# Optimization experiments

Measured on AMD Instinct MI355X. Metric: run time of the kernel, lower is better.

## Reference

```python
import jax, jax.numpy as jnp
import numpy as np
import math

N_HEADS = 16


def setup_inputs() -> dict:
    key = jax.random.key(0)
    ks = jax.random.split(key, 5)
    B, S, E = 2, 2048, 1024
    scale = 1.0 / math.sqrt(E)
    return {
        "x": jax.random.normal(ks[0], (B, S, E), dtype=jnp.float32),
        "w_in": jax.random.normal(ks[1], (3 * E, E), dtype=jnp.float32) * scale,
        "b_in": jax.random.normal(ks[2], (3 * E,), dtype=jnp.float32) * 0.01,
        "w_out": jax.random.normal(ks[3], (E, E), dtype=jnp.float32) * scale,
        "b_out": jax.random.normal(ks[4], (E,), dtype=jnp.float32) * 0.01,
    }


def reference(x, w_in, b_in, w_out, b_out):
    B, S, E = x.shape
    H = N_HEADS
    d = E // H
    # fused QKV projection: [B,S,3E]
    qkv = x @ w_in.T + b_in
    q, k, v = jnp.split(qkv, 3, axis=-1)
    # [B,S,E] -> [B,H,S,d]
    q = q.reshape(B, S, H, d).transpose(0, 2, 1, 3)
    k = k.reshape(B, S, H, d).transpose(0, 2, 1, 3)
    v = v.reshape(B, S, H, d).transpose(0, 2, 1, 3)
    # scores [B,H,S,S], scaled by 1/sqrt(d_head) (no causal mask: casual_mask=False)
    scores = jnp.einsum("bhqd,bhkd->bhqk", q, k) / jnp.sqrt(jnp.float32(d)).astype(x.dtype)
    w = jax.nn.softmax(scores, axis=-1)
    # attention output [B,H,S,d] -> [B,S,E]
    out = jnp.einsum("bhqk,bhkd->bhqd", w, v)
    out = out.transpose(0, 2, 1, 3).reshape(B, S, E)
    return out @ w_out.T + b_out
```

## Files before the change

kernel.cpp:

```cpp
#include <hip/hip_runtime.h>
#include <cstdint>


typedef __bf16 bf16x8 __attribute__((ext_vector_type(8)));
typedef short s16x4 __attribute__((ext_vector_type(4)));
typedef float f32x4 __attribute__((ext_vector_type(4)));

__device__ __forceinline__ unsigned short f32_to_bf16_rne(float f) {
    unsigned int u = __builtin_bit_cast(unsigned int, f);
    u += 0x7FFF + ((u >> 16) & 1);
    return (unsigned short)(u >> 16);
}

__device__ __forceinline__ unsigned int pack_bf16_trunc(float a, float b) {
    unsigned int ua = __builtin_bit_cast(unsigned int, a);
    unsigned int ub = __builtin_bit_cast(unsigned int, b);
    return __builtin_amdgcn_perm(ub, ua, 0x07060302u);
}

__device__ __forceinline__ void gload16(const void* g, void* l) {
    __builtin_amdgcn_global_load_lds(
        (const __attribute__((address_space(1))) unsigned int*)g,
        (__attribute__((address_space(3))) unsigned int*)l, 16, 0, 0);
}

__global__ void cvt_all(const float* __restrict__ x, const float* __restrict__ wi,
                        const float* __restrict__ wo, unsigned short* __restrict__ xb,
                        unsigned short* __restrict__ wib, unsigned short* __restrict__ wob) {
    int i = blockIdx.x * blockDim.x + threadIdx.x;
    const float* src; unsigned short* dst; int off;
    if (i < 1048576)            { src = x;  dst = xb;  off = i; }
    else if (i < 1048576 + 786432) { src = wi; dst = wib; off = i - 1048576; }
    else                        { src = wo; dst = wob; off = i - (1048576 + 786432); }
    float4 v = ((const float4*)src)[off];
    ushort4 o;
    o.x = f32_to_bf16_rne(v.x); o.y = f32_to_bf16_rne(v.y);
    o.z = f32_to_bf16_rne(v.z); o.w = f32_to_bf16_rne(v.w);
    ((ushort4*)dst)[off] = o;
}

__launch_bounds__(256)
__global__ void gemm_qkv(const unsigned short* __restrict__ X,
                         const unsigned short* __restrict__ W,
                         const float* __restrict__ bias,
                         unsigned short* __restrict__ Qp,
                         unsigned short* __restrict__ Kp,
                         unsigned short* __restrict__ Vt) {
    __shared__ __align__(16) unsigned short As[128 * 64];
    __shared__ __align__(16) unsigned short Bs[128 * 64];
    const int t = threadIdx.x;
    const int w = t >> 6, lane = t & 63, quad = lane >> 4, l16 = lane & 15;
    const int wm = (w >> 1) * 64, wn = (w & 1) * 64;
    const int m0 = blockIdx.y * 128, n0 = blockIdx.x * 128;

    f32x4 acc[4][4] = {};

    for (int kt = 0; kt < 1024; kt += 64) {
        __syncthreads();
#pragma unroll
        for (int i = 0; i < 4; ++i) {
            int c = t + 256 * i;
            int r = c >> 3, cc = (c & 7) * 8;
            gload16(&X[(m0 + r) * 1024 + kt + cc], &As[c * 8]);
            gload16(&W[(n0 + r) * 1024 + kt + cc], &Bs[c * 8]);
        }
        __syncthreads();
#pragma unroll
        for (int ks = 0; ks < 2; ++ks) {
            bf16x8 af[4], bw[4];
#pragma unroll
            for (int mi = 0; mi < 4; ++mi)
                af[mi] = *(const bf16x8*)&As[(wm + mi * 16 + l16) * 64 + ks * 32 + quad * 8];
#pragma unroll
            for (int ni = 0; ni < 4; ++ni)
                bw[ni] = *(const bf16x8*)&Bs[(wn + ni * 16 + l16) * 64 + ks * 32 + quad * 8];
#pragma unroll
            for (int mi = 0; mi < 4; ++mi)
#pragma unroll
                for (int ni = 0; ni < 4; ++ni)
                    acc[mi][ni] = __builtin_amdgcn_mfma_f32_16x16x32_bf16(af[mi], bw[ni], acc[mi][ni], 0, 0, 0);
        }
    }

    const float QSCALE = 0.125f * 1.44269504089f;
#pragma unroll
    for (int mi = 0; mi < 4; ++mi) {
#pragma unroll
        for (int ni = 0; ni < 4; ++ni) {
            int col = n0 + wn + ni * 16 + l16;
            float bv = bias[col];
            int which = col >> 10;
            int hc = col & 1023;
            int h = hc >> 6, d = hc & 63;
            int row0 = m0 + wm + mi * 16 + quad * 4;
            int b = row0 >> 11, s0 = row0 & 2047;
            int bh = b * 16 + h;
            if (which == 2) {
                ushort4 pk;
                pk.x = f32_to_bf16_rne(acc[mi][ni][0] + bv);
                pk.y = f32_to_bf16_rne(acc[mi][ni][1] + bv);
                pk.z = f32_to_bf16_rne(acc[mi][ni][2] + bv);
                pk.w = f32_to_bf16_rne(acc[mi][ni][3] + bv);
                *(ushort4*)&Vt[(bh * 64 + d) * 2048 + s0] = pk;
            } else if (which == 0) {
#pragma unroll
                for (int r = 0; r < 4; ++r)
                    Qp[(bh * 2048 + s0 + r) * 64 + d] =
                        f32_to_bf16_rne((acc[mi][ni][r] + bv) * QSCALE);
            } else {
#pragma unroll
                for (int r = 0; r < 4; ++r)
                    Kp[(bh * 2048 + s0 + r) * 64 + d] = f32_to_bf16_rne(acc[mi][ni][r] + bv);
            }
        }
    }
}

__launch_bounds__(256, 4)
__global__ void attn(const unsigned short* __restrict__ Qp, const unsigned short* __restrict__ Kp,
                     const unsigned short* __restrict__ Vt, unsigned short* __restrict__ A2) {
    __shared__ __align__(16) unsigned short Ks[2][64 * 64];
    __shared__ __align__(16) unsigned short Vs[2][64 * 64];
    const int t = threadIdx.x, lane = t & 63, quad = lane >> 4, l16 = lane & 15;
    const int w = t >> 6;
    const int wq = w & 1;
    const int wk = w >> 1;
    const int bh = blockIdx.x;
    const int qb = blockIdx.y;
    const unsigned short* Qh = Qp + bh * (2048 * 64);
    const unsigned short* Kh = Kp + bh * (2048 * 64);
    const unsigned short* Vh = Vt + bh * (64 * 2048);

    bf16x8 qf[2][2];
#pragma unroll
    for (int nq = 0; nq < 2; ++nq)
#pragma unroll
        for (int ks = 0; ks < 2; ++ks) {
            int row = qb * 64 + wq * 32 + nq * 16 + l16;
            qf[nq][ks] = *(const bf16x8*)&Qh[row * 64 + ks * 32 + quad * 8];
        }

    f32x4 o_acc[4][2] = {};
    float l_lane[2] = {0.f, 0.f};

#pragma unroll
    for (int i = 0; i < 2; ++i) {
        int c = t + 256 * i;
        int r = c >> 3, sc = ((c & 7) ^ (r & 7)) << 3;
        gload16(&Kh[r * 64 + sc], &Ks[0][c * 8]);
        gload16(&Vh[r * 2048 + sc], &Vs[0][c * 8]);
    }

    int cur = 0;
    for (int it = 0; it < 32; ++it) {
        __syncthreads();
        if (it != 31) {
            int ktn = (it + 1) * 64;
#pragma unroll
            for (int i = 0; i < 2; ++i) {
                int c = t + 256 * i;
                int r = c >> 3, sc = ((c & 7) ^ (r & 7)) << 3;
                gload16(&Kh[(ktn + r) * 64 + sc], &Ks[cur ^ 1][c * 8]);
                gload16(&Vh[r * 2048 + ktn + sc], &Vs[cur ^ 1][c * 8]);
            }
        }
        const unsigned short* Kc = Ks[cur];
        const unsigned short* Vc = Vs[cur];

        f32x4 s_acc[2][2] = {};
#pragma unroll
        for (int ks = 0; ks < 2; ++ks)
#pragma unroll
            for (int mi = 0; mi < 2; ++mi) {
                int row = wk * 32 + mi * 16 + l16;
                bf16x8 kf = *(const bf16x8*)&Kc[row * 64 +
                                                (((ks * 4 + quad) ^ (l16 & 7)) << 3)];
#pragma unroll
                for (int nq = 0; nq < 2; ++nq)
                    s_acc[mi][nq] = __builtin_amdgcn_mfma_f32_16x16x32_bf16(kf, qf[nq][ks], s_acc[mi][nq], 0, 0, 0);
            }

        s16x4 bq[2][2];
#pragma unroll
        for (int nq = 0; nq < 2; ++nq) {
            float rsum = 0.f;
#pragma unroll
            for (int mi = 0; mi < 2; ++mi) {
                float p0 = __builtin_amdgcn_exp2f(s_acc[mi][nq][0]);
                float p1 = __builtin_amdgcn_exp2f(s_acc[mi][nq][1]);
                float p2 = __builtin_amdgcn_exp2f(s_acc[mi][nq][2]);
                float p3 = __builtin_amdgcn_exp2f(s_acc[mi][nq][3]);
                rsum += (p0 + p1) + (p2 + p3);
                uint2 pk;
                pk.x = pack_bf16_trunc(p0, p1);
                pk.y = pack_bf16_trunc(p2, p3);
                bq[mi][nq] = __builtin_bit_cast(s16x4, pk);
            }
            l_lane[nq] += rsum;
        }

#pragma unroll
        for (int dm = 0; dm < 4; ++dm)
#pragma unroll
            for (int kt4 = 0; kt4 < 2; ++kt4) {
                int ch = (wk * 4 + kt4 * 2 + (quad >> 1)) ^ (l16 & 7);
                s16x4 av = __builtin_bit_cast(s16x4,
                    *(const uint2*)&Vc[(dm * 16 + l16) * 64 + (ch << 3) + (quad & 1) * 4]);
#pragma unroll
                for (int nq = 0; nq < 2; ++nq)
                    o_acc[dm][nq] = __builtin_amdgcn_mfma_f32_16x16x16bf16_1k(av, bq[kt4][nq], o_acc[dm][nq], 0, 0, 0);
            }
        cur ^= 1;
    }

    __syncthreads();
    float* fo = (float*)&Ks[0][0];
    float* fl = (float*)&Vs[0][0];
    if (wk == 1) {
#pragma unroll
        for (int nq = 0; nq < 2; ++nq) {
#pragma unroll
            for (int dm = 0; dm < 4; ++dm)
                *(f32x4*)&fo[(wq * 32 + nq * 16 + l16) * 64 + dm * 16 + quad * 4] = o_acc[dm][nq];
            fl[(wq * 2 + nq) * 64 + lane] = l_lane[nq];
        }
    }
    __syncthreads();
    if (wk == 0) {
        const int b = bh >> 4, h = bh & 15;
#pragma unroll
        for (int nq = 0; nq < 2; ++nq) {
#pragma unroll
            for (int dm = 0; dm < 4; ++dm)
                o_acc[dm][nq] += *(const f32x4*)&fo[(wq * 32 + nq * 16 + l16) * 64 + dm * 16 + quad * 4];
            float l = l_lane[nq] + fl[(wq * 2 + nq) * 64 + lane];
            l += __shfl_xor(l, 16);
            l += __shfl_xor(l, 32);
            float rl = 1.0f / l;
            int s = qb * 64 + wq * 32 + nq * 16 + l16;
            int tok = b * 2048 + s;
#pragma unroll
            for (int dm = 0; dm < 4; ++dm) {
                ushort4 o;
                o.x = f32_to_bf16_rne(o_acc[dm][nq][0] * rl);
                o.y = f32_to_bf16_rne(o_acc[dm][nq][1] * rl);
                o.z = f32_to_bf16_rne(o_acc[dm][nq][2] * rl);
                o.w = f32_to_bf16_rne(o_acc[dm][nq][3] * rl);
                *(ushort4*)&A2[tok * 1024 + h * 64 + dm * 16 + quad * 4] = o;
            }
        }
    }
}

__launch_bounds__(256)
__global__ void gemm_out_k(const unsigned short* __restrict__ A, const unsigned short* __restrict__ W,
                           const float* __restrict__ bias, float* __restrict__ out) {
    __shared__ __align__(16) unsigned short As[128 * 64];
    __shared__ __align__(16) unsigned short Bs[64 * 64];
    const int t = threadIdx.x;
    const int w = t >> 6, lane = t & 63, quad = lane >> 4, l16 = lane & 15;
    const int wm = (w >> 1) * 64, wn = (w & 1) * 32;
    const int m0 = blockIdx.y * 128, n0 = blockIdx.x * 64;

    f32x4 acc[4][2] = {};

    for (int kt = 0; kt < 1024; kt += 64) {
        __syncthreads();
#pragma unroll
        for (int i = 0; i < 4; ++i) {
            int c = t + 256 * i;
            int r = c >> 3, cc = (c & 7) * 8;
            gload16(&A[(m0 + r) * 1024 + kt + cc], &As[c * 8]);
        }
#pragma unroll
        for (int i = 0; i < 2; ++i) {
            int c = t + 256 * i;
            int r = c >> 3, cc = (c & 7) * 8;
            gload16(&W[(n0 + r) * 1024 + kt + cc], &Bs[c * 8]);
        }
        __syncthreads();
#pragma unroll
        for (int ks = 0; ks < 2; ++ks) {
            bf16x8 af[4], bw[2];
#pragma unroll
            for (int mi = 0; mi < 4; ++mi)
                af[mi] = *(const bf16x8*)&As[(wm + mi * 16 + l16) * 64 + ks * 32 + quad * 8];
#pragma unroll
            for (int ni = 0; ni < 2; ++ni)
                bw[ni] = *(const bf16x8*)&Bs[(wn + ni * 16 + l16) * 64 + ks * 32 + quad * 8];
#pragma unroll
            for (int mi = 0; mi < 4; ++mi)
#pragma unroll
                for (int ni = 0; ni < 2; ++ni)
                    acc[mi][ni] = __builtin_amdgcn_mfma_f32_16x16x32_bf16(af[mi], bw[ni], acc[mi][ni], 0, 0, 0);
        }
    }

#pragma unroll
    for (int mi = 0; mi < 4; ++mi)
#pragma unroll
        for (int ni = 0; ni < 2; ++ni) {
            int col = n0 + wn + ni * 16 + l16;
            float bv = bias[col];
#pragma unroll
            for (int r = 0; r < 4; ++r) {
                int row = m0 + wm + mi * 16 + quad * 4 + r;
                out[row * 1024 + col] = acc[mi][ni][r] + bv;
            }
        }
}

extern "C" void kernel_launch(void* const* d_in, const int* in_sizes, int n_in,
                              void* d_out, int out_size, void* d_ws, size_t ws_size,
                              hipStream_t stream) {
    const float* x     = (const float*)d_in[0];
    const float* w_in  = (const float*)d_in[1];
    const float* b_in  = (const float*)d_in[2];
    const float* w_out = (const float*)d_in[3];
    const float* b_out = (const float*)d_in[4];
    float* out = (float*)d_out;

    char* ws = (char*)d_ws;
    unsigned short* xb  = (unsigned short*)(ws);
    unsigned short* wib = (unsigned short*)(ws + 8388608);
    unsigned short* wob = (unsigned short*)(ws + 14680064);
    unsigned short* Qp  = (unsigned short*)(ws + 16777216);
    unsigned short* Kp  = (unsigned short*)(ws + 25165824);
    unsigned short* Vt  = (unsigned short*)(ws + 33554432);
    unsigned short* A2  = (unsigned short*)(ws + 41943040);

    cvt_all<<<8192, 256, 0, stream>>>(x, w_in, w_out, xb, wib, wob);
    gemm_qkv<<<dim3(24, 32), 256, 0, stream>>>(xb, wib, b_in, Qp, Kp, Vt);
    attn<<<dim3(32, 32), 256, 0, stream>>>(Qp, Kp, Vt, A2);
    gemm_out_k<<<dim3(16, 32), 256, 0, stream>>>(A2, wob, b_out, out);
}
```

Before: 200.0 us.

## Double-buffer LDS in both projection GEMMs and remap blocks per XCD

Both the QKV and output-projection GEMMs now use two LDS buffers with a K-step of 32. Each iteration prefetches the next tile through global_load_lds while the MFMAs run on the current tile, and only one barrier per step is needed. The launch grids are flattened to 1D and block indices are remapped so that each XCD works on a contiguous sub-grid, which is meant to improve L2 reuse of the shared A and W tiles. The smaller K-step means twice as many barriers and loop iterations, and overlap depends on the barrier's implicit vmcnt wait.

```diff
diff --git a/kernel.cpp b/kernel.cpp
--- a/kernel.cpp
+++ b/kernel.cpp
@@ -46,41 +46,56 @@
                          unsigned short* __restrict__ Qp,
                          unsigned short* __restrict__ Kp,
                          unsigned short* __restrict__ Vt) {
-    __shared__ __align__(16) unsigned short As[128 * 64];
-    __shared__ __align__(16) unsigned short Bs[128 * 64];
+    __shared__ __align__(16) unsigned short As[2][128 * 32];
+    __shared__ __align__(16) unsigned short Bs[2][128 * 32];
     const int t = threadIdx.x;
     const int w = t >> 6, lane = t & 63, quad = lane >> 4, l16 = lane & 15;
     const int wm = (w >> 1) * 64, wn = (w & 1) * 64;
-    const int m0 = blockIdx.y * 128, n0 = blockIdx.x * 128;
-
+    const int lin = blockIdx.x;
+    const int xcd = lin & 7, idx = lin >> 3;
+    const int bx = (xcd & 1) * 12 + idx % 12;
+    const int by = (xcd >> 1) * 8 + idx / 12;
+    const int m0 = by * 128, n0 = bx * 128;
+
+    const int sr = t >> 2, scc = (t & 3) * 8;
     f32x4 acc[4][4] = {};
 
-    for (int kt = 0; kt < 1024; kt += 64) {
+#pragma unroll
+    for (int i = 0; i < 2; ++i) {
+        int c = t + 256 * i;
+        int r = c >> 2, cc = (c & 3) * 8;
+        gload16(&X[(m0 + r) * 1024 + cc], &As[0][c * 8]);
+        gload16(&W[(n0 + r) * 1024 + cc], &Bs[0][c * 8]);
+    }
+
+    int cur = 0;
+    for (int kt = 0; kt < 1024; kt += 32) {
         __syncthreads();
-#pragma unroll
-        for (int i = 0; i < 4; ++i) {
-            int c = t + 256 * i;
-            int r = c >> 3, cc = (c & 7) * 8;
-            gload16(&X[(m0 + r) * 1024 + kt + cc], &As[c * 8]);
-            gload16(&W[(n0 + r) * 1024 + kt + cc], &Bs[c * 8]);
-        }
-        __syncthreads();
-#pragma unroll
-        for (int ks = 0; ks < 2; ++ks) {
-            bf16x8 af[4], bw[4];
-#pragma unroll
-            for (int mi = 0; mi < 4; ++mi)
-                af[mi] = *(const bf16x8*)&As[(wm + mi * 16 + l16) * 64 + ks * 32 + quad * 8];
+        if (kt != 992) {
+            int kn = kt + 32;
+#pragma unroll
+            for (int i = 0; i < 2; ++i) {
+                int c = t + 256 * i;
+                int r = c >> 2, cc = (c & 3) * 8;
+                gload16(&X[(m0 + r) * 1024 + kn + cc], &As[cur ^ 1][c * 8]);
+                gload16(&W[(n0 + r) * 1024 + kn + cc], &Bs[cur ^ 1][c * 8]);
+            }
+        }
+        bf16x8 af[4], bw[4];
+#pragma unroll
+        for (int mi = 0; mi < 4; ++mi)
+            af[mi] = *(const bf16x8*)&As[cur][(wm + mi * 16 + l16) * 32 + quad * 8];
+#pragma unroll
+        for (int ni = 0; ni < 4; ++ni)
+            bw[ni] = *(const bf16x8*)&Bs[cur][(wn + ni * 16 + l16) * 32 + quad * 8];
+#pragma unroll
+        for (int mi = 0; mi < 4; ++mi)
 #pragma unroll
             for (int ni = 0; ni < 4; ++ni)
-                bw[ni] = *(const bf16x8*)&Bs[(wn + ni * 16 + l16) * 64 + ks * 32 + quad * 8];
-#pragma unroll
-            for (int mi = 0; mi < 4; ++mi)
-#pragma unroll
-                for (int ni = 0; ni < 4; ++ni)
-                    acc[mi][ni] = __builtin_amdgcn_mfma_f32_16x16x32_bf16(af[mi], bw[ni], acc[mi][ni], 0, 0, 0);
-        }
-    }
+                acc[mi][ni] = __builtin_amdgcn_mfma_f32_16x16x32_bf16(af[mi], bw[ni], acc[mi][ni], 0, 0, 0);
+        cur ^= 1;
+    }
+    (void)sr; (void)scc;
 
     const float QSCALE = 0.125f * 1.44269504089f;
 #pragma unroll
@@ -255,45 +270,57 @@
 __launch_bounds__(256)
 __global__ void gemm_out_k(const unsigned short* __restrict__ A, const unsigned short* __restrict__ W,
                            const float* __restrict__ bias, float* __restrict__ out) {
-    __shared__ __align__(16) unsigned short As[128 * 64];
-    __shared__ __align__(16) unsigned short Bs[64 * 64];
+    __shared__ __align__(16) unsigned short As[2][128 * 32];
+    __shared__ __align__(16) unsigned short Bs[2][64 * 32];
     const int t = threadIdx.x;
     const int w = t >> 6, lane = t & 63, quad = lane >> 4, l16 = lane & 15;
     const int wm = (w >> 1) * 64, wn = (w & 1) * 32;
-    const int m0 = blockIdx.y * 128, n0 = blockIdx.x * 64;
+    const int lin = blockIdx.x;
+    const int xcd = lin & 7, idx = lin >> 3;
+    const int bx = (xcd & 1) * 8 + idx % 8;
+    const int by = (xcd >> 1) * 8 + idx / 8;
+    const int m0 = by * 128, n0 = bx * 64;
 
     f32x4 acc[4][2] = {};
 
-    for (int kt = 0; kt < 1024; kt += 64) {
-        __syncthreads();
-#pragma unroll
-        for (int i = 0; i < 4; ++i) {
-            int c = t + 256 * i;
-            int r = c >> 3, cc = (c & 7) * 8;
-            gload16(&A[(m0 + r) * 1024 + kt + cc], &As[c * 8]);
-        }
+    {
 #pragma unroll
         for (int i = 0; i < 2; ++i) {
             int c = t + 256 * i;
-            int r = c >> 3, cc = (c & 7) * 8;
-            gload16(&W[(n0 + r) * 1024 + kt + cc], &Bs[c * 8]);
-        }
+            int r = c >> 2, cc = (c & 3) * 8;
+            gload16(&A[(m0 + r) * 1024 + cc], &As[0][c * 8]);
+        }
+        int r = t >> 2, cc = (t & 3) * 8;
+        gload16(&W[(n0 + r) * 1024 + cc], &Bs[0][t * 8]);
+    }
+
+    int cur = 0;
+    for (int kt = 0; kt < 1024; kt += 32) {
         __syncthreads();
-#pragma unroll
-        for (int ks = 0; ks < 2; ++ks) {
-            bf16x8 af[4], bw[2];
-#pragma unroll
-            for (int mi = 0; mi < 4; ++mi)
-                af[mi] = *(const bf16x8*)&As[(wm + mi * 16 + l16) * 64 + ks * 32 + quad * 8];
+        if (kt != 992) {
+            int kn = kt + 32;
+#pragma unroll
+            for (int i = 0; i < 2; ++i) {
+                int c = t + 256 * i;
+                int r = c >> 2, cc = (c & 3) * 8;
+                gload16(&A[(m0 + r) * 1024 + kn + cc], &As[cur ^ 1][c * 8]);
+            }
+            int r = t >> 2, cc = (t & 3) * 8;
+            gload16(&W[(n0 + r) * 1024 + kn + cc], &Bs[cur ^ 1][t * 8]);
+        }
+        bf16x8 af[4], bw[2];
+#pragma unroll
+        for (int mi = 0; mi < 4; ++mi)
+            af[mi] = *(const bf16x8*)&As[cur][(wm + mi * 16 + l16) * 32 + quad * 8];
+#pragma unroll
+        for (int ni = 0; ni < 2; ++ni)
+            bw[ni] = *(const bf16x8*)&Bs[cur][(wn + ni * 16 + l16) * 32 + quad * 8];
+#pragma unroll
+        for (int mi = 0; mi < 4; ++mi)
 #pragma unroll
             for (int ni = 0; ni < 2; ++ni)
-                bw[ni] = *(const bf16x8*)&Bs[(wn + ni * 16 + l16) * 64 + ks * 32 + quad * 8];
-#pragma unroll
-            for (int mi = 0; mi < 4; ++mi)
-#pragma unroll
-                for (int ni = 0; ni < 2; ++ni)
-                    acc[mi][ni] = __builtin_amdgcn_mfma_f32_16x16x32_bf16(af[mi], bw[ni], acc[mi][ni], 0, 0, 0);
-        }
+                acc[mi][ni] = __builtin_amdgcn_mfma_f32_16x16x32_bf16(af[mi], bw[ni], acc[mi][ni], 0, 0, 0);
+        cur ^= 1;
     }
 
 #pragma unroll
@@ -330,7 +357,7 @@
     unsigned short* A2  = (unsigned short*)(ws + 41943040);
 
     cvt_all<<<8192, 256, 0, stream>>>(x, w_in, w_out, xb, wib, wob);
-    gemm_qkv<<<dim3(24, 32), 256, 0, stream>>>(xb, wib, b_in, Qp, Kp, Vt);
+    gemm_qkv<<<768, 256, 0, stream>>>(xb, wib, b_in, Qp, Kp, Vt);
     attn<<<dim3(32, 32), 256, 0, stream>>>(Qp, Kp, Vt, A2);
-    gemm_out_k<<<dim3(16, 32), 256, 0, stream>>>(A2, wob, b_out, out);
-}
+    gemm_out_k<<<512, 256, 0, stream>>>(A2, wob, b_out, out);
+}
```

Measured after the change: 198.9 us. No clear change (-0.6%).

## Triple-buffer GEMM K-loop with async LDS loads and XCD-aware block remap

Applied to the files above, without the earlier changes.

Both projection GEMMs switch from a single-buffered 64-wide K tile with two barriers per step to a three-stage ring of 32-wide K tiles. Global-to-LDS loads run two stages ahead, with vmcnt waits and one barrier per step, so loads overlap MFMA work. Blocks are remapped so that the blocks sharing an XCD cover a contiguous region of the output tile grid, which should improve L2 reuse. The output GEMM also shrinks its tiles to 64x64 to launch more blocks, at the cost of less reuse per block and more loop iterations.

```diff
diff --git a/kernel.cpp b/kernel.cpp
--- a/kernel.cpp
+++ b/kernel.cpp
@@ -46,41 +46,57 @@
                          unsigned short* __restrict__ Qp,
                          unsigned short* __restrict__ Kp,
                          unsigned short* __restrict__ Vt) {
-    __shared__ __align__(16) unsigned short As[128 * 64];
-    __shared__ __align__(16) unsigned short Bs[128 * 64];
+    __shared__ __align__(16) unsigned short As[3][128 * 32];
+    __shared__ __align__(16) unsigned short Bs[3][128 * 32];
     const int t = threadIdx.x;
     const int w = t >> 6, lane = t & 63, quad = lane >> 4, l16 = lane & 15;
     const int wm = (w >> 1) * 64, wn = (w & 1) * 64;
-    const int m0 = blockIdx.y * 128, n0 = blockIdx.x * 128;
+    const int lin = blockIdx.x;
+    const int xcd = lin & 7, idx = lin >> 3;
+    const int bx = (xcd & 1) * 12 + idx % 12;
+    const int by = (xcd >> 1) * 8 + idx / 12;
+    const int m0 = by * 128, n0 = bx * 128;
+
+    const int c0 = t, c1 = t + 256;
+    const int r0 = c0 >> 2, cc0 = (c0 & 3) * 8;
+    const int r1 = c1 >> 2, cc1 = (c1 & 3) * 8;
+#define QKV_STAGE(kt, buf)                                             \
+    do {                                                               \
+        gload16(&X[(m0 + r0) * 1024 + (kt) + cc0], &As[buf][c0 * 8]);  \
+        gload16(&W[(n0 + r0) * 1024 + (kt) + cc0], &Bs[buf][c0 * 8]);  \
+        gload16(&X[(m0 + r1) * 1024 + (kt) + cc1], &As[buf][c1 * 8]);  \
+        gload16(&W[(n0 + r1) * 1024 + (kt) + cc1], &Bs[buf][c1 * 8]);  \
+    } while (0)
 
     f32x4 acc[4][4] = {};
 
-    for (int kt = 0; kt < 1024; kt += 64) {
-        __syncthreads();
-#pragma unroll
-        for (int i = 0; i < 4; ++i) {
-            int c = t + 256 * i;
-            int r = c >> 3, cc = (c & 7) * 8;
-            gload16(&X[(m0 + r) * 1024 + kt + cc], &As[c * 8]);
-            gload16(&W[(n0 + r) * 1024 + kt + cc], &Bs[c * 8]);
-        }
-        __syncthreads();
-#pragma unroll
-        for (int ks = 0; ks < 2; ++ks) {
-            bf16x8 af[4], bw[4];
-#pragma unroll
-            for (int mi = 0; mi < 4; ++mi)
-                af[mi] = *(const bf16x8*)&As[(wm + mi * 16 + l16) * 64 + ks * 32 + quad * 8];
+    QKV_STAGE(0, 0);
+    QKV_STAGE(32, 1);
+
+    int cur = 0, nxt = 1, nn = 2;
+    for (int k = 0; k < 32; ++k) {
+        if (k == 31) { asm volatile("s_waitcnt vmcnt(0)" ::: "memory"); }
+        else         { asm volatile("s_waitcnt vmcnt(4)" ::: "memory"); }
+        __builtin_amdgcn_s_barrier();
+        asm volatile("" ::: "memory");
+        if (k < 30) QKV_STAGE((k + 2) * 32, nn);
+        const unsigned short* Ab = As[cur];
+        const unsigned short* Bb = Bs[cur];
+        bf16x8 af[4], bw[4];
+#pragma unroll
+        for (int mi = 0; mi < 4; ++mi)
+            af[mi] = *(const bf16x8*)&Ab[(wm + mi * 16 + l16) * 32 + quad * 8];
+#pragma unroll
+        for (int ni = 0; ni < 4; ++ni)
+            bw[ni] = *(const bf16x8*)&Bb[(wn + ni * 16 + l16) * 32 + quad * 8];
+#pragma unroll
+        for (int mi = 0; mi < 4; ++mi)
 #pragma unroll
             for (int ni = 0; ni < 4; ++ni)
-                bw[ni] = *(const bf16x8*)&Bs[(wn + ni * 16 + l16) * 64 + ks * 32 + quad * 8];
-#pragma unroll
-            for (int mi = 0; mi < 4; ++mi)
-#pragma unroll
-                for (int ni = 0; ni < 4; ++ni)
-                    acc[mi][ni] = __builtin_amdgcn_mfma_f32_16x16x32_bf16(af[mi], bw[ni], acc[mi][ni], 0, 0, 0);
-        }
-    }
+                acc[mi][ni] = __builtin_amdgcn_mfma_f32_16x16x32_bf16(af[mi], bw[ni], acc[mi][ni], 0, 0, 0);
+        int tmp = cur; cur = nxt; nxt = nn; nn = tmp;
+    }
+#undef QKV_STAGE
 
     const float QSCALE = 0.125f * 1.44269504089f;
 #pragma unroll
@@ -255,49 +271,56 @@
 __launch_bounds__(256)
 __global__ void gemm_out_k(const unsigned short* __restrict__ A, const unsigned short* __restrict__ W,
                            const float* __restrict__ bias, float* __restrict__ out) {
-    __shared__ __align__(16) unsigned short As[128 * 64];
-    __shared__ __align__(16) unsigned short Bs[64 * 64];
+    __shared__ __align__(16) unsigned short As[3][64 * 32];
+    __shared__ __align__(16) unsigned short Bs[3][64 * 32];
     const int t = threadIdx.x;
     const int w = t >> 6, lane = t & 63, quad = lane >> 4, l16 = lane & 15;
-    const int wm = (w >> 1) * 64, wn = (w & 1) * 32;
-    const int m0 = blockIdx.y * 128, n0 = blockIdx.x * 64;
-
-    f32x4 acc[4][2] = {};
-
-    for (int kt = 0; kt < 1024; kt += 64) {
-        __syncthreads();
-#pragma unroll
-        for (int i = 0; i < 4; ++i) {
-            int c = t + 256 * i;
-            int r = c >> 3, cc = (c & 7) * 8;
-            gload16(&A[(m0 + r) * 1024 + kt + cc], &As[c * 8]);
-        }
-#pragma unroll
-        for (int i = 0; i < 2; ++i) {
-            int c = t + 256 * i;
-            int r = c >> 3, cc = (c & 7) * 8;
-            gload16(&W[(n0 + r) * 1024 + kt + cc], &Bs[c * 8]);
-        }
-        __syncthreads();
-#pragma unroll
-        for (int ks = 0; ks < 2; ++ks) {
-            bf16x8 af[4], bw[2];
-#pragma unroll
-            for (int mi = 0; mi < 4; ++mi)
-                af[mi] = *(const bf16x8*)&As[(wm + mi * 16 + l16) * 64 + ks * 32 + quad * 8];
+    const int wm = (w >> 1) * 32, wn = (w & 1) * 32;
+    const int lin = blockIdx.x;
+    const int xcd = lin & 7, idx = lin >> 3;
+    const int bx = (xcd & 1) * 8 + idx % 8;
+    const int by = (xcd >> 1) * 16 + idx / 8;
+    const int m0 = by * 64, n0 = bx * 64;
+
+    const int r0 = t >> 2, cc0 = (t & 3) * 8;
+#define OUT_STAGE(kt, buf)                                             \
+    do {                                                               \
+        gload16(&A[(m0 + r0) * 1024 + (kt) + cc0], &As[buf][t * 8]);   \
+        gload16(&W[(n0 + r0) * 1024 + (kt) + cc0], &Bs[buf][t * 8]);   \
+    } while (0)
+
+    f32x4 acc[2][2] = {};
+
+    OUT_STAGE(0, 0);
+    OUT_STAGE(32, 1);
+
+    int cur = 0, nxt = 1, nn = 2;
+    for (int k = 0; k < 32; ++k) {
+        if (k == 31) { asm volatile("s_waitcnt vmcnt(0)" ::: "memory"); }
+        else         { asm volatile("s_waitcnt vmcnt(2)" ::: "memory"); }
+        __builtin_amdgcn_s_barrier();
+        asm volatile("" ::: "memory");
+        if (k < 30) OUT_STAGE((k + 2) * 32, nn);
+        const unsigned short* Ab = As[cur];
+        const unsigned short* Bb = Bs[cur];
+        bf16x8 af[2], bw[2];
+#pragma unroll
+        for (int mi = 0; mi < 2; ++mi)
+            af[mi] = *(const bf16x8*)&Ab[(wm + mi * 16 + l16) * 32 + quad * 8];
+#pragma unroll
+        for (int ni = 0; ni < 2; ++ni)
+            bw[ni] = *(const bf16x8*)&Bb[(wn + ni * 16 + l16) * 32 + quad * 8];
+#pragma unroll
+        for (int mi = 0; mi < 2; ++mi)
 #pragma unroll
             for (int ni = 0; ni < 2; ++ni)
-                bw[ni] = *(const bf16x8*)&Bs[(wn + ni * 16 + l16) * 64 + ks * 32 + quad * 8];
-#pragma unroll
-            for (int mi = 0; mi < 4; ++mi)
-#pragma unroll
-                for (int ni = 0; ni < 2; ++ni)
-                    acc[mi][ni] = __builtin_amdgcn_mfma_f32_16x16x32_bf16(af[mi], bw[ni], acc[mi][ni], 0, 0, 0);
-        }
-    }
-
-#pragma unroll
-    for (int mi = 0; mi < 4; ++mi)
+                acc[mi][ni] = __builtin_amdgcn_mfma_f32_16x16x32_bf16(af[mi], bw[ni], acc[mi][ni], 0, 0, 0);
+        int tmp = cur; cur = nxt; nxt = nn; nn = tmp;
+    }
+#undef OUT_STAGE
+
+#pragma unroll
+    for (int mi = 0; mi < 2; ++mi)
 #pragma unroll
         for (int ni = 0; ni < 2; ++ni) {
             int col = n0 + wn + ni * 16 + l16;
@@ -330,7 +353,7 @@
     unsigned short* A2  = (unsigned short*)(ws + 41943040);
 
     cvt_all<<<8192, 256, 0, stream>>>(x, w_in, w_out, xb, wib, wob);
-    gemm_qkv<<<dim3(24, 32), 256, 0, stream>>>(xb, wib, b_in, Qp, Kp, Vt);
+    gemm_qkv<<<768, 256, 0, stream>>>(xb, wib, b_in, Qp, Kp, Vt);
     attn<<<dim3(32, 32), 256, 0, stream>>>(Qp, Kp, Vt, A2);
-    gemm_out_k<<<dim3(16, 32), 256, 0, stream>>>(A2, wob, b_out, out);
-}
+    gemm_out_k<<<1024, 256, 0, stream>>>(A2, wob, b_out, out);
+}
```

Result: faster. 192.3 us (-3.9%).
